# Performance work log

Measured on AMD Instinct MI355X. Metric: run time of the kernel, lower is better.

Reference implementation:

```python
import jax, jax.numpy as jnp
import numpy as np

VOCAB = 21
SEQ_DIM = 128
HIDDEN = 1024
HEADS = 16
LAYERS = 6
B, S = 4, 2048
EPS = 1e-5


def _layer_norm(x, g, b):
    mu = jnp.mean(x, axis=-1, keepdims=True)
    var = jnp.mean(jnp.square(x - mu), axis=-1, keepdims=True)
    return (x - mu) * jax.lax.rsqrt(var + EPS) * g + b


def setup_inputs() -> dict:
    key = jax.random.key(0)
    ks = jax.random.split(key, 16)
    sc = 0.02
    D = HIDDEN
    inp = {
        "sequences": jax.random.randint(ks[0], (B, S), 0, VOCAB, dtype=jnp.int64)
        if jax.config.jax_enable_x64 else jax.random.randint(ks[0], (B, S), 0, VOCAB, dtype=jnp.int32),
        "mask": jnp.ones((B, S), dtype=jnp.int32),
        "emb": jax.random.normal(ks[1], (VOCAB, SEQ_DIM), jnp.float32) * sc,
        "proj_w": jax.random.normal(ks[2], (SEQ_DIM, D), jnp.float32) * sc,
        "proj_b": jnp.zeros((D,), jnp.float32),
        "qw": jax.random.normal(ks[3], (LAYERS, D, D), jnp.float32) * sc,
        "qb": jnp.zeros((LAYERS, D), jnp.float32),
        "kw": jax.random.normal(ks[4], (LAYERS, D, D), jnp.float32) * sc,
        "kb": jnp.zeros((LAYERS, D), jnp.float32),
        "vw": jax.random.normal(ks[5], (LAYERS, D, D), jnp.float32) * sc,
        "vb": jnp.zeros((LAYERS, D), jnp.float32),
        "ow": jax.random.normal(ks[6], (LAYERS, D, D), jnp.float32) * sc,
        "ob": jnp.zeros((LAYERS, D), jnp.float32),
        "ln_g": jnp.ones((LAYERS, D), jnp.float32),
        "ln_b": jnp.zeros((LAYERS, D), jnp.float32),
    }
    return inp


def reference(sequences, mask, emb, proj_w, proj_b, qw, qb, kw, kb, vw, vb, ow, ob, ln_g, ln_b):
    hd = HIDDEN // HEADS
    scale = 1.0 / np.sqrt(hd).astype(np.float32)
    # embedding lookup + projection
    x = emb[sequences]                      # [B,S,SEQ_DIM]
    x = x @ proj_w + proj_b                 # [B,S,D]
    neg = jnp.float32(-1e9)
    mbool = (mask == 0)[:, None, None, :]   # [B,1,1,S]
    for l in range(LAYERS):
        q = (x @ qw[l] + qb[l]).reshape(B, S, HEADS, hd)
        k = (x @ kw[l] + kb[l]).reshape(B, S, HEADS, hd)
        v = (x @ vw[l] + vb[l]).reshape(B, S, HEADS, hd)
        scores = jnp.einsum("bqhd,bkhd->bhqk", q, k) * scale
        scores = jnp.where(mbool, neg, scores)
        attn = jax.nn.softmax(scores, axis=-1)  # dropout is identity in eval
        out = jnp.einsum("bhqk,bkhd->bqhd", attn, v).reshape(B, S, HIDDEN)
        out = out @ ow[l] + ob[l]
        x = _layer_norm(x + out, ln_g[l], ln_b[l])
    return x
```

## Files before the change

kernel.cpp:

```cpp
#include <hip/hip_runtime.h>
#include <hip/hip_bf16.h>

#define D 1024
#define NTOK 8192
#define SEQ 2048
#define NB 4
#define NH 16
#define HD 64
#define NLAYER 6

typedef __attribute__((ext_vector_type(8))) short short8;
typedef __attribute__((ext_vector_type(4))) float f32x4;
typedef __attribute__((ext_vector_type(16))) float f32x16;
typedef unsigned short u16;
typedef unsigned int uint;

__device__ __forceinline__ u16 f2bf(float f) {
  __hip_bfloat16 h = __float2bfloat16(f);
  return *reinterpret_cast<u16*>(&h);
}

__device__ __forceinline__ uint pkbf(float a, float b) {
  return (uint)f2bf(a) | ((uint)f2bf(b) << 16);
}

__device__ __forceinline__ float ex2(float x) {
  float r;
  asm("v_exp_f32 %0, %1" : "=v"(r) : "v"(x));
  return r;
}

__device__ __forceinline__ void gld16(void* lds, const void* g) {
  __builtin_amdgcn_global_load_lds(
      (const __attribute__((address_space(1))) unsigned int*)g,
      (__attribute__((address_space(3))) unsigned int*)lds, 16, 0, 0);
}

__global__ __launch_bounds__(1024) void wconv_kernel(
    const float* __restrict__ qw, const float* __restrict__ kw,
    const float* __restrict__ vw, const float* __restrict__ ow,
    __hip_bfloat16* __restrict__ wT) {
  __shared__ float tile[32][33];
  const int z = blockIdx.z;
  const int t = z & 3;
  const float* src = (t == 0) ? qw : (t == 1) ? kw : (t == 2) ? vw : ow;
  src += (size_t)(z >> 2) * (D * D);
  __hip_bfloat16* dst = wT + (size_t)z * (D * D);
  const int k = blockIdx.y * 32 + threadIdx.y;
  const int n = blockIdx.x * 32 + threadIdx.x;
  tile[threadIdx.y][threadIdx.x] = src[(size_t)k * D + n];
  __syncthreads();
  const int nn = blockIdx.x * 32 + threadIdx.y;
  const int kk = blockIdx.y * 32 + threadIdx.x;
  dst[(size_t)nn * D + kk] = __float2bfloat16(tile[threadIdx.x][threadIdx.y]);
}

__global__ __launch_bounds__(256) void vproj_kernel(
    const float* __restrict__ emb, const float* __restrict__ pw,
    const float* __restrict__ pb, float* __restrict__ tab) {
  __shared__ float e[128];
  const int v = blockIdx.y;
  const int d = blockIdx.x * 256 + threadIdx.x;
  if (threadIdx.x < 128) e[threadIdx.x] = emb[v * 128 + threadIdx.x];
  __syncthreads();
  float acc = pb[d];
  #pragma unroll 8
  for (int kk = 0; kk < 128; ++kk) acc += e[kk] * pw[kk * D + d];
  tab[v * D + d] = acc;
}

__global__ __launch_bounds__(256) void gather_kernel(
    const int* __restrict__ seq, const float* __restrict__ tab,
    float* __restrict__ x, __hip_bfloat16* __restrict__ xb) {
  const int t = blockIdx.x;
  const int v = seq[t];
  const int c = threadIdx.x * 4;
  f32x4 tv = *(const f32x4*)(tab + v * D + c);
  *(f32x4*)(x + (size_t)t * D + c) = tv;
  union { u16 u[4]; uint2 q; } pk;
  #pragma unroll
  for (int j = 0; j < 4; ++j) pk.u[j] = f2bf(tv[j]);
  *(uint2*)(xb + (size_t)t * D + c) = pk.q;
}

template <int MODE>
__global__ __launch_bounds__(256) void gemm_kernel(
    const __hip_bfloat16* __restrict__ A, const __hip_bfloat16* __restrict__ Bt,
    const float* __restrict__ bias, __hip_bfloat16* __restrict__ obf,
    float* __restrict__ of32) {
  __shared__ __hip_bfloat16 lA[128][32];
  __shared__ __hip_bfloat16 lB[128][32];
  const int tid = threadIdx.x;
  const int w = tid >> 6, l = tid & 63;
  const int m0 = blockIdx.y * 128, n0 = blockIdx.x * 128;
  const int gr = tid >> 2, gc = (tid & 3) * 8;
  const __hip_bfloat16* ga = A + (size_t)(m0 + gr) * D + gc;
  const __hip_bfloat16* gb = Bt + (size_t)(n0 + gr) * D + gc;
  char* lab = (char*)&lA[0][0] + w * 1024;
  char* lbb = (char*)&lB[0][0] + w * 1024;
  const int wm = (w >> 1) * 64, wn = (w & 1) * 64;
  const int fr = l & 15, fk = (l >> 4) * 8;
  f32x4 acc[4][4] = {};

  for (int k0 = 0; k0 < D; k0 += 32) {
    if (k0) __syncthreads();
    gld16(lab, ga + k0);
    gld16(lab + 4096, ga + (size_t)64 * D + k0);
    gld16(lbb, gb + k0);
    gld16(lbb + 4096, gb + (size_t)64 * D + k0);
    __syncthreads();
    short8 af[4], bf[4];
    #pragma unroll
    for (int mi = 0; mi < 4; ++mi) af[mi] = *(const short8*)&lA[wm + mi * 16 + fr][fk];
    #pragma unroll
    for (int ni = 0; ni < 4; ++ni) bf[ni] = *(const short8*)&lB[wn + ni * 16 + fr][fk];
    #pragma unroll
    for (int mi = 0; mi < 4; ++mi)
      #pragma unroll
      for (int ni = 0; ni < 4; ++ni)
        acc[mi][ni] = __builtin_amdgcn_mfma_f32_16x16x32_bf16(af[mi], bf[ni], acc[mi][ni], 0, 0, 0);
  }

  #pragma unroll
  for (int mi = 0; mi < 4; ++mi) {
    #pragma unroll
    for (int ni = 0; ni < 4; ++ni) {
      const int row = m0 + wm + mi * 16 + (l >> 4) * 4;
      const int col = n0 + wn + ni * 16 + fr;
      const float bv = bias[col];
      if (MODE == 0) {
        #pragma unroll
        for (int j = 0; j < 4; ++j)
          obf[(size_t)(row + j) * D + col] = __float2bfloat16(acc[mi][ni][j] + bv);
      } else if (MODE == 1) {
        const int bb = row >> 11, s = row & (SEQ - 1);
        union { u16 u[4]; uint2 q; } pk;
        #pragma unroll
        for (int j = 0; j < 4; ++j) pk.u[j] = f2bf(acc[mi][ni][j] + bv);
        *(uint2*)(obf + ((size_t)(bb * D + col)) * SEQ + s) = pk.q;
      } else {
        #pragma unroll
        for (int j = 0; j < 4; ++j) {
          const size_t idx = (size_t)(row + j) * D + col;
          of32[idx] = of32[idx] + acc[mi][ni][j] + bv;
        }
      }
    }
  }
}

__global__ __launch_bounds__(256, 4) void attn_kernel(
    const __hip_bfloat16* __restrict__ Q, const __hip_bfloat16* __restrict__ Kb,
    const __hip_bfloat16* __restrict__ Vt, const int* __restrict__ mask,
    __hip_bfloat16* __restrict__ O) {
  __shared__ float lmask[SEQ];
  __shared__ __hip_bfloat16 lKV[2][2][64][64];

  const int tid = threadIdx.x;
  const int w = tid >> 6, l = tid & 63;
  const int lo = l & 31, hi = l >> 5;
  const int x7 = lo & 7;
  const int b = blockIdx.z, h = blockIdx.y;
  const int q0 = blockIdx.x * 128 + w * 32;
  const float S2 = 0.18033688f;

  #pragma unroll
  for (int i = 0; i < 8; ++i) {
    const int idx = tid + i * 256;
    lmask[idx] = mask[b * SEQ + idx] ? 0.f : -30000.f;
  }

  const __hip_bfloat16* gq = Q + ((size_t)(b * SEQ + q0 + lo)) * D + h * HD + hi * 8;
  short8 qf[4];
  #pragma unroll
  for (int c = 0; c < 4; ++c) qf[c] = *(const short8*)(gq + c * 16);

  const int r0 = w * 8 + (l >> 3);
  const int sK = (l & 7) ^ (r0 & 7);
  const __hip_bfloat16* gk0 = Kb + ((size_t)(b * SEQ + r0)) * D + h * HD + sK * 8;
  const __hip_bfloat16* gv0 = Vt + ((size_t)(b * D + h * HD + r0)) * SEQ + sK * 8;
  char* const kb0 = (char*)&lKV[0][0][0][0];
  char* const vb0 = (char*)&lKV[0][1][0][0];
  char* const kb1 = (char*)&lKV[1][0][0][0];
  char* const vb1 = (char*)&lKV[1][1][0][0];

#define STAGE(T, BUF) do {                                                  \
    char* kb_ = (BUF) ? kb1 : kb0;                                          \
    char* vb_ = (BUF) ? vb1 : vb0;                                          \
    gld16(kb_ + w * 1024,        gk0 + (size_t)(T) * 64 * D);               \
    gld16(kb_ + 4096 + w * 1024, gk0 + (size_t)(T) * 64 * D + 32 * (size_t)D); \
    gld16(vb_ + w * 1024,        gv0 + (T) * 64);                           \
    gld16(vb_ + 4096 + w * 1024, gv0 + (size_t)32 * SEQ + (T) * 64);        \
  } while (0)

  STAGE(0, 0);
  __syncthreads();

  float m_run = -3e38f, l_run = 0.f;
  f32x16 oacc[2] = {};

  for (int t = 0; t < SEQ / 64; ++t) {
    const int cur = t & 1;
    if (t + 1 < SEQ / 64) STAGE(t + 1, cur ^ 1);
    const char* KR = cur ? kb1 : kb0;
    const char* VR = cur ? vb1 : vb0;

    #pragma unroll
    for (int kvs = 0; kvs < 2; ++kvs) {
      f32x16 pf = {};
      #pragma unroll
      for (int c = 0; c < 4; ++c) {
        short8 kf = *(const short8*)(KR + kvs * 4096 + lo * 128 + (((2 * c + hi) ^ x7) << 4));
        pf = __builtin_amdgcn_mfma_f32_32x32x16_bf16(kf, qf[c], pf, 0, 0, 0);
      }
      const float* mrow = lmask + t * 64 + kvs * 32 + hi * 4;
      f32x4 mq[4];
      #pragma unroll
      for (int g = 0; g < 4; ++g) mq[g] = *(const f32x4*)(mrow + g * 8);

      float mx = -3e38f;
      #pragma unroll
      for (int r = 0; r < 16; ++r)
        mx = fmaxf(mx, __builtin_fmaf(pf[r], S2, mq[r >> 2][r & 3]));
      mx = fmaxf(mx, __shfl_xor(mx, 32));

      if (!__all(mx <= m_run + 8.f)) {
        const float mn = fmaxf(m_run, mx);
        const float fs = ex2(m_run - mn);
        l_run *= fs;
        #pragma unroll
        for (int dt = 0; dt < 2; ++dt)
          #pragma unroll
          for (int r = 0; r < 16; ++r) oacc[dt][r] *= fs;
        m_run = mn;
      }

      float p[16];
      float ls = 0.f;
      #pragma unroll
      for (int r = 0; r < 16; ++r) {
        p[r] = ex2(__builtin_fmaf(pf[r], S2, mq[r >> 2][r & 3]) - m_run);
        ls += p[r];
      }
      ls += __shfl_xor(ls, 32);
      l_run += ls;

      uint w0a = pkbf(p[0], p[1]),   w1a = pkbf(p[2], p[3]);
      uint w0b = pkbf(p[4], p[5]),   w1b = pkbf(p[6], p[7]);
      uint w2a = pkbf(p[8], p[9]),   w3a = pkbf(p[10], p[11]);
      uint w2b = pkbf(p[12], p[13]), w3b = pkbf(p[14], p[15]);
      asm volatile("v_permlane32_swap_b32 %0, %1" : "+v"(w0a), "+v"(w0b));
      asm volatile("v_permlane32_swap_b32 %0, %1" : "+v"(w1a), "+v"(w1b));
      asm volatile("v_permlane32_swap_b32 %0, %1" : "+v"(w2a), "+v"(w2b));
      asm volatile("v_permlane32_swap_b32 %0, %1" : "+v"(w3a), "+v"(w3b));
      union { uint u[4]; short8 s; } pu0, pu1;
      pu0.u[0] = w0a; pu0.u[1] = w1a; pu0.u[2] = w0b; pu0.u[3] = w1b;
      pu1.u[0] = w2a; pu1.u[1] = w3a; pu1.u[2] = w2b; pu1.u[3] = w3b;

      #pragma unroll
      for (int dt = 0; dt < 2; ++dt) {
        short8 vf0 = *(const short8*)(VR + dt * 4096 + lo * 128 + (((kvs * 4 + hi) ^ x7) << 4));
        oacc[dt] = __builtin_amdgcn_mfma_f32_32x32x16_bf16(vf0, pu0.s, oacc[dt], 0, 0, 0);
        short8 vf1 = *(const short8*)(VR + dt * 4096 + lo * 128 + (((kvs * 4 + 2 + hi) ^ x7) << 4));
        oacc[dt] = __builtin_amdgcn_mfma_f32_32x32x16_bf16(vf1, pu1.s, oacc[dt], 0, 0, 0);
      }
    }
    __syncthreads();
  }
#undef STAGE

  const float rl = 1.f / l_run;
  __hip_bfloat16* orow = O + ((size_t)(b * SEQ + q0 + lo)) * D + h * HD;
  #pragma unroll
  for (int dt = 0; dt < 2; ++dt)
    #pragma unroll
    for (int g = 0; g < 4; ++g) {
      union { u16 u[4]; uint2 q2; } pk4;
      #pragma unroll
      for (int j = 0; j < 4; ++j) pk4.u[j] = f2bf(oacc[dt][g * 4 + j] * rl);
      *(uint2*)(orow + dt * 32 + g * 8 + hi * 4) = pk4.q2;
    }
}

__global__ __launch_bounds__(256) void ln_kernel(
    float* __restrict__ x, const float* __restrict__ g,
    const float* __restrict__ bt, __hip_bfloat16* __restrict__ xb) {
  __shared__ float red[10];
  const int row = blockIdx.x;
  const int c = threadIdx.x * 4;
  f32x4 v = *(const f32x4*)(x + (size_t)row * D + c);
  float s = v[0] + v[1] + v[2] + v[3];
  float ss = v[0] * v[0] + v[1] * v[1] + v[2] * v[2] + v[3] * v[3];
  #pragma unroll
  for (int o = 32; o; o >>= 1) { s += __shfl_xor(s, o); ss += __shfl_xor(ss, o); }
  const int w = threadIdx.x >> 6, l = threadIdx.x & 63;
  if (l == 0) { red[w] = s; red[4 + w] = ss; }
  __syncthreads();
  if (threadIdx.x == 0) {
    const float S = red[0] + red[1] + red[2] + red[3];
    const float SS = red[4] + red[5] + red[6] + red[7];
    const float mu = S * (1.f / D);
    const float var = SS * (1.f / D) - mu * mu;
    red[8] = mu;
    red[9] = 1.f / sqrtf(var + 1e-5f);
  }
  __syncthreads();
  const float mu = red[8], rs = red[9];
  f32x4 gv = *(const f32x4*)(g + c);
  f32x4 bv = *(const f32x4*)(bt + c);
  f32x4 o;
  union { u16 u[4]; uint2 q; } pk;
  #pragma unroll
  for (int j = 0; j < 4; ++j) {
    o[j] = (v[j] - mu) * rs * gv[j] + bv[j];
    pk.u[j] = f2bf(o[j]);
  }
  *(f32x4*)(x + (size_t)row * D + c) = o;
  *(uint2*)(xb + (size_t)row * D + c) = pk.q;
}

extern "C" void kernel_launch(void* const* d_in, const int* in_sizes, int n_in,
                              void* d_out, int out_size, void* d_ws, size_t ws_size,
                              hipStream_t stream) {
  const int* seq = (const int*)d_in[0];
  const int* mask = (const int*)d_in[1];
  const float* emb = (const float*)d_in[2];
  const float* pw = (const float*)d_in[3];
  const float* pb = (const float*)d_in[4];
  const float* qw = (const float*)d_in[5];
  const float* qb = (const float*)d_in[6];
  const float* kw = (const float*)d_in[7];
  const float* kb = (const float*)d_in[8];
  const float* vw = (const float*)d_in[9];
  const float* vb = (const float*)d_in[10];
  const float* ow = (const float*)d_in[11];
  const float* ob = (const float*)d_in[12];
  const float* lng = (const float*)d_in[13];
  const float* lnb = (const float*)d_in[14];
  float* xout = (float*)d_out;

  char* ws = (char*)d_ws;
  __hip_bfloat16* wT = (__hip_bfloat16*)ws;
  float* tab = (float*)(ws + 50331648);
  __hip_bfloat16* xb = (__hip_bfloat16*)(ws + 50462720);
  __hip_bfloat16* qs = (__hip_bfloat16*)(ws + 67239936);
  __hip_bfloat16* ks = (__hip_bfloat16*)(ws + 84017152);
  __hip_bfloat16* vt = (__hip_bfloat16*)(ws + 100794368);
  __hip_bfloat16* ao = (__hip_bfloat16*)(ws + 117571584);

  wconv_kernel<<<dim3(32, 32, 24), dim3(32, 32), 0, stream>>>(qw, kw, vw, ow, wT);
  vproj_kernel<<<dim3(4, 21), 256, 0, stream>>>(emb, pw, pb, tab);
  gather_kernel<<<NTOK, 256, 0, stream>>>(seq, tab, xout, xb);

  for (int lyr = 0; lyr < NLAYER; ++lyr) {
    const __hip_bfloat16* wq = wT + (size_t)(lyr * 4 + 0) * D * D;
    const __hip_bfloat16* wk = wT + (size_t)(lyr * 4 + 1) * D * D;
    const __hip_bfloat16* wv = wT + (size_t)(lyr * 4 + 2) * D * D;
    const __hip_bfloat16* wo = wT + (size_t)(lyr * 4 + 3) * D * D;
    gemm_kernel<0><<<dim3(8, 64), 256, 0, stream>>>(xb, wq, qb + lyr * D, qs, nullptr);
    gemm_kernel<0><<<dim3(8, 64), 256, 0, stream>>>(xb, wk, kb + lyr * D, ks, nullptr);
    gemm_kernel<1><<<dim3(8, 64), 256, 0, stream>>>(xb, wv, vb + lyr * D, vt, nullptr);
    attn_kernel<<<dim3(16, 16, 4), 256, 0, stream>>>(qs, ks, vt, mask, ao);
    gemm_kernel<2><<<dim3(8, 64), 256, 0, stream>>>(ao, wo, ob + lyr * D, nullptr, xout);
    ln_kernel<<<NTOK, 256, 0, stream>>>(xout, lng + lyr * D, lnb + lyr * D, xb);
  }
}
```

Before: 1.739 ms.

## Fuse QKV projections into one GEMM and restructure attention softmax loop

```diff
diff --git a/kernel.cpp b/kernel.cpp
--- a/kernel.cpp
+++ b/kernel.cpp
@@ -14,6 +14,8 @@
 typedef __attribute__((ext_vector_type(16))) float f32x16;
 typedef unsigned short u16;
 typedef unsigned int uint;
+
+#define S2L 0.18033688011112042f
 
 __device__ __forceinline__ u16 f2bf(float f) {
   __hip_bfloat16 h = __float2bfloat16(f);
@@ -83,11 +85,76 @@
   *(uint2*)(xb + (size_t)t * D + c) = pk.q;
 }
 
-template <int MODE>
-__global__ __launch_bounds__(256) void gemm_kernel(
+__global__ __launch_bounds__(256) void gemm_qkv_kernel(
     const __hip_bfloat16* __restrict__ A, const __hip_bfloat16* __restrict__ Bt,
-    const float* __restrict__ bias, __hip_bfloat16* __restrict__ obf,
-    float* __restrict__ of32) {
+    const float* __restrict__ qb, const float* __restrict__ kbias,
+    const float* __restrict__ vbias, __hip_bfloat16* __restrict__ qs,
+    __hip_bfloat16* __restrict__ ks, __hip_bfloat16* __restrict__ vt) {
+  __shared__ __hip_bfloat16 lA[128][32];
+  __shared__ __hip_bfloat16 lB[128][32];
+  const int tid = threadIdx.x;
+  const int w = tid >> 6, l = tid & 63;
+  const int m0 = blockIdx.y * 128, n0 = blockIdx.x * 128;
+  const int which = blockIdx.x >> 3;
+  const int gr = tid >> 2, gc = (tid & 3) * 8;
+  const __hip_bfloat16* ga = A + (size_t)(m0 + gr) * D + gc;
+  const __hip_bfloat16* gb = Bt + (size_t)(n0 + gr) * D + gc;
+  char* lab = (char*)&lA[0][0] + w * 1024;
+  char* lbb = (char*)&lB[0][0] + w * 1024;
+  const int wm = (w >> 1) * 64, wn = (w & 1) * 64;
+  const int fr = l & 15, fk = (l >> 4) * 8;
+  f32x4 acc[4][4] = {};
+
+  for (int k0 = 0; k0 < D; k0 += 32) {
+    if (k0) __syncthreads();
+    gld16(lab, ga + k0);
+    gld16(lab + 4096, ga + (size_t)64 * D + k0);
+    gld16(lbb, gb + k0);
+    gld16(lbb + 4096, gb + (size_t)64 * D + k0);
+    __syncthreads();
+    short8 af[4], bf[4];
+    #pragma unroll
+    for (int mi = 0; mi < 4; ++mi) af[mi] = *(const short8*)&lA[wm + mi * 16 + fr][fk];
+    #pragma unroll
+    for (int ni = 0; ni < 4; ++ni) bf[ni] = *(const short8*)&lB[wn + ni * 16 + fr][fk];
+    #pragma unroll
+    for (int mi = 0; mi < 4; ++mi)
+      #pragma unroll
+      for (int ni = 0; ni < 4; ++ni)
+        acc[mi][ni] = __builtin_amdgcn_mfma_f32_16x16x32_bf16(af[mi], bf[ni], acc[mi][ni], 0, 0, 0);
+  }
+
+  #pragma unroll
+  for (int mi = 0; mi < 4; ++mi) {
+    #pragma unroll
+    for (int ni = 0; ni < 4; ++ni) {
+      const int row = m0 + wm + mi * 16 + (l >> 4) * 4;
+      const int col = (n0 + wn + ni * 16 + fr) & 1023;
+      if (which == 0) {
+        const float bv = qb[col];
+        #pragma unroll
+        for (int j = 0; j < 4; ++j)
+          qs[(size_t)(row + j) * D + col] = __float2bfloat16((acc[mi][ni][j] + bv) * S2L);
+      } else if (which == 1) {
+        const float bv = kbias[col];
+        #pragma unroll
+        for (int j = 0; j < 4; ++j)
+          ks[(size_t)(row + j) * D + col] = __float2bfloat16(acc[mi][ni][j] + bv);
+      } else {
+        const float bv = vbias[col];
+        const int bb = row >> 11, s = row & (SEQ - 1);
+        union { u16 u[4]; uint2 q; } pk;
+        #pragma unroll
+        for (int j = 0; j < 4; ++j) pk.u[j] = f2bf(acc[mi][ni][j] + bv);
+        *(uint2*)(vt + ((size_t)(bb * D + col)) * SEQ + s) = pk.q;
+      }
+    }
+  }
+}
+
+__global__ __launch_bounds__(256) void gemm_o_kernel(
+    const __hip_bfloat16* __restrict__ A, const __hip_bfloat16* __restrict__ Bt,
+    const float* __restrict__ bias, float* __restrict__ of32) {
   __shared__ __hip_bfloat16 lA[128][32];
   __shared__ __hip_bfloat16 lB[128][32];
   const int tid = threadIdx.x;
@@ -128,22 +195,10 @@
       const int row = m0 + wm + mi * 16 + (l >> 4) * 4;
       const int col = n0 + wn + ni * 16 + fr;
       const float bv = bias[col];
-      if (MODE == 0) {
-        #pragma unroll
-        for (int j = 0; j < 4; ++j)
-          obf[(size_t)(row + j) * D + col] = __float2bfloat16(acc[mi][ni][j] + bv);
-      } else if (MODE == 1) {
-        const int bb = row >> 11, s = row & (SEQ - 1);
-        union { u16 u[4]; uint2 q; } pk;
-        #pragma unroll
-        for (int j = 0; j < 4; ++j) pk.u[j] = f2bf(acc[mi][ni][j] + bv);
-        *(uint2*)(obf + ((size_t)(bb * D + col)) * SEQ + s) = pk.q;
-      } else {
-        #pragma unroll
-        for (int j = 0; j < 4; ++j) {
-          const size_t idx = (size_t)(row + j) * D + col;
-          of32[idx] = of32[idx] + acc[mi][ni][j] + bv;
-        }
+      #pragma unroll
+      for (int j = 0; j < 4; ++j) {
+        const size_t idx = (size_t)(row + j) * D + col;
+        of32[idx] = of32[idx] + acc[mi][ni][j] + bv;
       }
     }
   }
@@ -153,7 +208,7 @@
     const __hip_bfloat16* __restrict__ Q, const __hip_bfloat16* __restrict__ Kb,
     const __hip_bfloat16* __restrict__ Vt, const int* __restrict__ mask,
     __hip_bfloat16* __restrict__ O) {
-  __shared__ float lmask[SEQ];
+  __shared__ unsigned char lmu8[SEQ];
   __shared__ __hip_bfloat16 lKV[2][2][64][64];
 
   const int tid = threadIdx.x;
@@ -162,12 +217,11 @@
   const int x7 = lo & 7;
   const int b = blockIdx.z, h = blockIdx.y;
   const int q0 = blockIdx.x * 128 + w * 32;
-  const float S2 = 0.18033688f;
 
   #pragma unroll
   for (int i = 0; i < 8; ++i) {
     const int idx = tid + i * 256;
-    lmask[idx] = mask[b * SEQ + idx] ? 0.f : -30000.f;
+    lmu8[idx] = mask[b * SEQ + idx] ? 1 : 0;
   }
 
   const __hip_bfloat16* gq = Q + ((size_t)(b * SEQ + q0 + lo)) * D + h * HD + hi * 8;
@@ -205,50 +259,71 @@
     const char* KR = cur ? kb1 : kb0;
     const char* VR = cur ? vb1 : vb0;
 
-    #pragma unroll
-    for (int kvs = 0; kvs < 2; ++kvs) {
-      f32x16 pf = {};
-      #pragma unroll
-      for (int c = 0; c < 4; ++c) {
-        short8 kf = *(const short8*)(KR + kvs * 4096 + lo * 128 + (((2 * c + hi) ^ x7) << 4));
-        pf = __builtin_amdgcn_mfma_f32_32x32x16_bf16(kf, qf[c], pf, 0, 0, 0);
+    f32x16 pf0 = {}, pf1 = {};
+    __builtin_amdgcn_s_setprio(1);
+    #pragma unroll
+    for (int c = 0; c < 4; ++c) {
+      short8 kf0 = *(const short8*)(KR + lo * 128 + (((2 * c + hi) ^ x7) << 4));
+      pf0 = __builtin_amdgcn_mfma_f32_32x32x16_bf16(kf0, qf[c], pf0, 0, 0, 0);
+      short8 kf1 = *(const short8*)(KR + 4096 + lo * 128 + (((2 * c + hi) ^ x7) << 4));
+      pf1 = __builtin_amdgcn_mfma_f32_32x32x16_bf16(kf1, qf[c], pf1, 0, 0, 0);
+    }
+    __builtin_amdgcn_s_setprio(0);
+
+    const unsigned char mv = lmu8[t * 64 + l];
+    if (!__all(mv != 0)) {
+      #pragma unroll
+      for (int r = 0; r < 16; ++r) {
+        const int kv = (r & 3) + 8 * (r >> 2) + 4 * hi;
+        if (!lmu8[t * 64 + kv]) pf0[r] = -1e5f;
+        if (!lmu8[t * 64 + 32 + kv]) pf1[r] = -1e5f;
       }
-      const float* mrow = lmask + t * 64 + kvs * 32 + hi * 4;
-      f32x4 mq[4];
-      #pragma unroll
-      for (int g = 0; g < 4; ++g) mq[g] = *(const f32x4*)(mrow + g * 8);
-
-      float mx = -3e38f;
-      #pragma unroll
-      for (int r = 0; r < 16; ++r)
-        mx = fmaxf(mx, __builtin_fmaf(pf[r], S2, mq[r >> 2][r & 3]));
-      mx = fmaxf(mx, __shfl_xor(mx, 32));
-
-      if (!__all(mx <= m_run + 8.f)) {
-        const float mn = fmaxf(m_run, mx);
-        const float fs = ex2(m_run - mn);
-        l_run *= fs;
+    }
+
+    float mm[16];
+    #pragma unroll
+    for (int r = 0; r < 16; ++r) mm[r] = fmaxf(pf0[r], pf1[r]);
+    #pragma unroll
+    for (int s = 8; s; s >>= 1)
+      #pragma unroll
+      for (int r = 0; r < 8; ++r)
+        if (r < s) mm[r] = fmaxf(mm[r], mm[r + s]);
+    float ma = mm[0], mb2 = mm[0];
+    asm volatile("v_permlane32_swap_b32 %0, %1" : "+v"(ma), "+v"(mb2));
+    const float mx = fmaxf(ma, mb2);
+
+    if (!__all(mx <= m_run + 8.f)) {
+      const float mn = fmaxf(m_run, mx);
+      const float fs = ex2(m_run - mn);
+      l_run *= fs;
+      #pragma unroll
+      for (int dt = 0; dt < 2; ++dt)
         #pragma unroll
-        for (int dt = 0; dt < 2; ++dt)
-          #pragma unroll
-          for (int r = 0; r < 16; ++r) oacc[dt][r] *= fs;
-        m_run = mn;
-      }
-
-      float p[16];
-      float ls = 0.f;
-      #pragma unroll
-      for (int r = 0; r < 16; ++r) {
-        p[r] = ex2(__builtin_fmaf(pf[r], S2, mq[r >> 2][r & 3]) - m_run);
-        ls += p[r];
-      }
-      ls += __shfl_xor(ls, 32);
-      l_run += ls;
-
-      uint w0a = pkbf(p[0], p[1]),   w1a = pkbf(p[2], p[3]);
-      uint w0b = pkbf(p[4], p[5]),   w1b = pkbf(p[6], p[7]);
-      uint w2a = pkbf(p[8], p[9]),   w3a = pkbf(p[10], p[11]);
-      uint w2b = pkbf(p[12], p[13]), w3b = pkbf(p[14], p[15]);
+        for (int r = 0; r < 16; ++r) oacc[dt][r] *= fs;
+      m_run = mn;
+    }
+
+    float p0[16], p1[16];
+    #pragma unroll
+    for (int r = 0; r < 16; ++r) {
+      p0[r] = ex2(pf0[r] - m_run);
+      p1[r] = ex2(pf1[r] - m_run);
+    }
+    float sm[16];
+    #pragma unroll
+    for (int r = 0; r < 16; ++r) sm[r] = p0[r] + p1[r];
+    #pragma unroll
+    for (int s = 8; s; s >>= 1)
+      #pragma unroll
+      for (int r = 0; r < 8; ++r)
+        if (r < s) sm[r] += sm[r + s];
+    l_run += sm[0];
+
+    {
+      uint w0a = pkbf(p0[0], p0[1]),   w1a = pkbf(p0[2], p0[3]);
+      uint w0b = pkbf(p0[4], p0[5]),   w1b = pkbf(p0[6], p0[7]);
+      uint w2a = pkbf(p0[8], p0[9]),   w3a = pkbf(p0[10], p0[11]);
+      uint w2b = pkbf(p0[12], p0[13]), w3b = pkbf(p0[14], p0[15]);
       asm volatile("v_permlane32_swap_b32 %0, %1" : "+v"(w0a), "+v"(w0b));
       asm volatile("v_permlane32_swap_b32 %0, %1" : "+v"(w1a), "+v"(w1b));
       asm volatile("v_permlane32_swap_b32 %0, %1" : "+v"(w2a), "+v"(w2b));
@@ -256,20 +331,45 @@
       union { uint u[4]; short8 s; } pu0, pu1;
       pu0.u[0] = w0a; pu0.u[1] = w1a; pu0.u[2] = w0b; pu0.u[3] = w1b;
       pu1.u[0] = w2a; pu1.u[1] = w3a; pu1.u[2] = w2b; pu1.u[3] = w3b;
-
+      __builtin_amdgcn_s_setprio(1);
       #pragma unroll
       for (int dt = 0; dt < 2; ++dt) {
-        short8 vf0 = *(const short8*)(VR + dt * 4096 + lo * 128 + (((kvs * 4 + hi) ^ x7) << 4));
+        short8 vf0 = *(const short8*)(VR + dt * 4096 + lo * 128 + (((hi) ^ x7) << 4));
         oacc[dt] = __builtin_amdgcn_mfma_f32_32x32x16_bf16(vf0, pu0.s, oacc[dt], 0, 0, 0);
-        short8 vf1 = *(const short8*)(VR + dt * 4096 + lo * 128 + (((kvs * 4 + 2 + hi) ^ x7) << 4));
+        short8 vf1 = *(const short8*)(VR + dt * 4096 + lo * 128 + (((2 + hi) ^ x7) << 4));
         oacc[dt] = __builtin_amdgcn_mfma_f32_32x32x16_bf16(vf1, pu1.s, oacc[dt], 0, 0, 0);
       }
+      __builtin_amdgcn_s_setprio(0);
+    }
+    {
+      uint w0a = pkbf(p1[0], p1[1]),   w1a = pkbf(p1[2], p1[3]);
+      uint w0b = pkbf(p1[4], p1[5]),   w1b = pkbf(p1[6], p1[7]);
+      uint w2a = pkbf(p1[8], p1[9]),   w3a = pkbf(p1[10], p1[11]);
+      uint w2b = pkbf(p1[12], p1[13]), w3b = pkbf(p1[14], p1[15]);
+      asm volatile("v_permlane32_swap_b32 %0, %1" : "+v"(w0a), "+v"(w0b));
+      asm volatile("v_permlane32_swap_b32 %0, %1" : "+v"(w1a), "+v"(w1b));
+      asm volatile("v_permlane32_swap_b32 %0, %1" : "+v"(w2a), "+v"(w2b));
+      asm volatile("v_permlane32_swap_b32 %0, %1" : "+v"(w3a), "+v"(w3b));
+      union { uint u[4]; short8 s; } pu0, pu1;
+      pu0.u[0] = w0a; pu0.u[1] = w1a; pu0.u[2] = w0b; pu0.u[3] = w1b;
+      pu1.u[0] = w2a; pu1.u[1] = w3a; pu1.u[2] = w2b; pu1.u[3] = w3b;
+      __builtin_amdgcn_s_setprio(1);
+      #pragma unroll
+      for (int dt = 0; dt < 2; ++dt) {
+        short8 vf0 = *(const short8*)(VR + dt * 4096 + lo * 128 + (((4 + hi) ^ x7) << 4));
+        oacc[dt] = __builtin_amdgcn_mfma_f32_32x32x16_bf16(vf0, pu0.s, oacc[dt], 0, 0, 0);
+        short8 vf1 = *(const short8*)(VR + dt * 4096 + lo * 128 + (((6 + hi) ^ x7) << 4));
+        oacc[dt] = __builtin_amdgcn_mfma_f32_32x32x16_bf16(vf1, pu1.s, oacc[dt], 0, 0, 0);
+      }
+      __builtin_amdgcn_s_setprio(0);
     }
     __syncthreads();
   }
 #undef STAGE
 
-  const float rl = 1.f / l_run;
+  float la = l_run, lb2 = l_run;
+  asm volatile("v_permlane32_swap_b32 %0, %1" : "+v"(la), "+v"(lb2));
+  const float rl = 1.f / (la + lb2);
   __hip_bfloat16* orow = O + ((size_t)(b * SEQ + q0 + lo)) * D + h * HD;
   #pragma unroll
   for (int dt = 0; dt < 2; ++dt)
@@ -353,15 +453,12 @@
   gather_kernel<<<NTOK, 256, 0, stream>>>(seq, tab, xout, xb);
 
   for (int lyr = 0; lyr < NLAYER; ++lyr) {
-    const __hip_bfloat16* wq = wT + (size_t)(lyr * 4 + 0) * D * D;
-    const __hip_bfloat16* wk = wT + (size_t)(lyr * 4 + 1) * D * D;
-    const __hip_bfloat16* wv = wT + (size_t)(lyr * 4 + 2) * D * D;
+    const __hip_bfloat16* wTl = wT + (size_t)(lyr * 4) * D * D;
     const __hip_bfloat16* wo = wT + (size_t)(lyr * 4 + 3) * D * D;
-    gemm_kernel<0><<<dim3(8, 64), 256, 0, stream>>>(xb, wq, qb + lyr * D, qs, nullptr);
-    gemm_kernel<0><<<dim3(8, 64), 256, 0, stream>>>(xb, wk, kb + lyr * D, ks, nullptr);
-    gemm_kernel<1><<<dim3(8, 64), 256, 0, stream>>>(xb, wv, vb + lyr * D, vt, nullptr);
+    gemm_qkv_kernel<<<dim3(24, 64), 256, 0, stream>>>(
+        xb, wTl, qb + lyr * D, kb + lyr * D, vb + lyr * D, qs, ks, vt);
     attn_kernel<<<dim3(16, 16, 4), 256, 0, stream>>>(qs, ks, vt, mask, ao);
-    gemm_kernel<2><<<dim3(8, 64), 256, 0, stream>>>(ao, wo, ob + lyr * D, nullptr, xout);
+    gemm_o_kernel<<<dim3(8, 64), 256, 0, stream>>>(ao, wo, ob + lyr * D, xout);
     ln_kernel<<<NTOK, 256, 0, stream>>>(xout, lng + lyr * D, lnb + lyr * D, xb);
   }
 }
```

New measurement: 1.559 ms. -10.4%, faster.
